# Optimization experiments

Hardware: AMD Instinct MI355X
Metric: run time of the kernel (lower is better)

Reference implementation:

```python
import jax, jax.numpy as jnp
import numpy as np

B, T, D, L, M = 32, 512, 512, 1024, 10


def setup_inputs() -> dict:
    key = jax.random.key(0)
    ks = jax.random.split(key, 9)
    s = 1.0 / np.sqrt(D)  # torch default uniform init bound
    u = lambda k, sh: jax.random.uniform(k, sh, jnp.float32, -s, s)
    return {
        "input_h_c": jax.random.normal(ks[0], (B, T, D), jnp.float32),
        "memory": jax.random.normal(ks[1], (B, L, D), jnp.float32),
        "input_lengths": jax.random.randint(ks[2], (B,), 1, L + 1),
        "W_ih": u(ks[3], (4 * D, 2 * D)),
        "W_hh": u(ks[4], (4 * D, D)),
        "b_ih": u(ks[5], (4 * D,)),
        "b_hh": u(ks[6], (4 * D,)),
        "W_g": u(ks[7], (3 * M, D)),
        "b_g": u(ks[8], (3 * M,)),
    }


def reference(input_h_c, memory, input_lengths, W_ih, W_hh, b_ih, b_hh, W_g, b_g):
    Bq, Tq, Dq = input_h_c.shape
    Lq = memory.shape[1]
    Mq = b_g.shape[0] // 3
    u_pos = jnp.arange(Lq, dtype=memory.dtype)  # [L]

    def step(carry, x_t):
        h, c, ctx, _ = carry
        x = jnp.concatenate([x_t, ctx], axis=-1)  # [B, 2D]
        gates = x @ W_ih.T + b_ih + h @ W_hh.T + b_hh  # [B, 4D]
        i, f, g, o = jnp.split(gates, 4, axis=-1)  # torch LSTMCell gate order i,f,g,o
        c_n = jax.nn.sigmoid(f) * c + jax.nn.sigmoid(i) * jnp.tanh(g)
        h_n = jax.nn.sigmoid(o) * jnp.tanh(c_n)
        # GMM CDF location attention
        phi = h_n @ W_g.T + b_g  # [B, 3M]
        ksi = jnp.exp(phi[:, :Mq])
        beta = jnp.exp(phi[:, Mq:2 * Mq])
        alpha = jax.nn.softmax(phi[:, 2 * Mq:], axis=-1)
        # 1/(1+exp((ksi-u)/beta)) == sigmoid((u-ksi)/beta)
        cdf = lambda ub: jnp.sum(
            alpha[..., None] * jax.nn.sigmoid((ub - ksi[..., None]) / beta[..., None]),
            axis=1)  # [B, L]
        t1 = cdf(u_pos + 0.5)
        w = t1 - cdf(u_pos - 0.5)  # [B, L]
        ctx_n = jnp.einsum('bl,bld->bd', w, memory)
        return (h_n, c_n, ctx_n, 1.0 - t1), w

    z = jnp.zeros((Bq, Dq), input_h_c.dtype)
    term0 = jnp.zeros((Bq, Lq), input_h_c.dtype)
    (h, c, ctx, term), ws = jax.lax.scan(step, (z, z, z, term0),
                                         jnp.swapaxes(input_h_c, 0, 1))
    alignment = jnp.swapaxes(ws, 0, 1)  # [B, T, L]
    termination = jnp.take_along_axis(term, (input_lengths - 1)[:, None], axis=1)  # [B,1]
    return ctx[:, None, :], alignment, termination
```

## Files before the change

kernel.cpp:

```cpp
#include <hip/hip_runtime.h>

#define Bz 32
#define Tz 512
#define Dz 512
#define Lz 1024
#define Mz 10
#define G4D 2048
#define FP 32
#define NBLKA 32
#define NBLK 64
#define OFF_FG   0
#define OFF_FH   1024
#define OFF_FC   2048
#define OFF_SC   3072
#define OFF_SH   11264
#define OFF_PART 19456
#define OFF_XW   84992
#define PM 128
#define PN 128
#define PK 32

typedef unsigned long long u64;
typedef unsigned u32;
typedef _Float16 f16x8 __attribute__((ext_vector_type(8)));
typedef float f32x4 __attribute__((ext_vector_type(4)));
typedef _Float16 half2_t __attribute__((ext_vector_type(2)));

__device__ __forceinline__ float fsig(float x) { return 1.0f / (1.0f + __expf(-x)); }
__device__ __forceinline__ int ld_rlx(const int* p) {
  return __hip_atomic_load(p, __ATOMIC_RELAXED, __HIP_MEMORY_SCOPE_AGENT);
}
__device__ __forceinline__ void st_rlx(int* p, int v) {
  __hip_atomic_store(p, v, __ATOMIC_RELAXED, __HIP_MEMORY_SCOPE_AGENT);
}
__device__ __forceinline__ void st_rlxu(u32* p, u32 v) {
  __hip_atomic_store(p, v, __ATOMIC_RELAXED, __HIP_MEMORY_SCOPE_AGENT);
}
__device__ __forceinline__ u64 ld_rlx64(const u64* p) {
  return __hip_atomic_load(p, __ATOMIC_RELAXED, __HIP_MEMORY_SCOPE_AGENT);
}
__device__ __forceinline__ u32 pack16(float a, float b) {
  unsigned short la = __builtin_bit_cast(unsigned short, (_Float16)a);
  unsigned short lb = __builtin_bit_cast(unsigned short, (_Float16)b);
  return (u32)la | ((u32)lb << 16);
}
#define VWAIT() asm volatile("s_waitcnt vmcnt(0)" ::: "memory")

__global__ __launch_bounds__(256) void k_pre(
    const float* __restrict__ x, const float* __restrict__ W_ih,
    const float* __restrict__ b_ih, const float* __restrict__ b_hh,
    float* __restrict__ xw)
{
  __shared__ float As[PM][PK+1];
  __shared__ float Bs[PN][PK+1];
  const int m0 = blockIdx.x*PM, n0 = blockIdx.y*PN;
  const int tid = threadIdx.x;
  const int mg = tid >> 4, ng = tid & 15;
  float acc[8][8] = {};
  for (int k0 = 0; k0 < Dz; k0 += PK) {
    for (int i = tid; i < PM*(PK/4); i += 256) {
      int row = i >> 3, c4 = (i & 7) << 2;
      float4 v = *reinterpret_cast<const float4*>(&x[(size_t)(m0+row)*Dz + k0 + c4]);
      As[row][c4] = v.x; As[row][c4+1] = v.y; As[row][c4+2] = v.z; As[row][c4+3] = v.w;
    }
    for (int i = tid; i < PN*(PK/4); i += 256) {
      int row = i >> 3, c4 = (i & 7) << 2;
      float4 v = *reinterpret_cast<const float4*>(&W_ih[(size_t)(n0+row)*(2*Dz) + k0 + c4]);
      Bs[row][c4] = v.x; Bs[row][c4+1] = v.y; Bs[row][c4+2] = v.z; Bs[row][c4+3] = v.w;
    }
    __syncthreads();
    #pragma unroll 8
    for (int k = 0; k < PK; k++) {
      float a8[8], b8[8];
      #pragma unroll
      for (int r = 0; r < 8; r++) a8[r] = As[mg*8+r][k];
      #pragma unroll
      for (int s = 0; s < 8; s++) b8[s] = Bs[ng*8+s][k];
      #pragma unroll
      for (int r = 0; r < 8; r++)
        #pragma unroll
        for (int s = 0; s < 8; s++) acc[r][s] += a8[r]*b8[s];
    }
    __syncthreads();
  }
  #pragma unroll
  for (int r = 0; r < 8; r++) {
    int m = m0 + mg*8 + r;
    #pragma unroll
    for (int s = 0; s < 8; s++) {
      int n = n0 + ng*8 + s;
      xw[(size_t)m*G4D + n] = acc[r][s] + b_ih[n] + b_hh[n];
    }
  }
}

__global__ __launch_bounds__(512, 1) void k_persist(
    const float* __restrict__ memory, const int* __restrict__ lens,
    const float* __restrict__ W_ih, const float* __restrict__ W_hh,
    const float* __restrict__ W_g,  const float* __restrict__ b_g,
    const float* __restrict__ xw,
    u32* __restrict__ stat_c, u32* __restrict__ stat_h, u32* __restrict__ part,
    int* __restrict__ fG, int* __restrict__ fH, int* __restrict__ fC,
    float* __restrict__ ctx_out, float* __restrict__ align_out,
    float* __restrict__ term_out)
{
  const int blk = blockIdx.x, tid = threadIdx.x;
  __shared__ __align__(16) char smem[149760];
  __shared__ float phis[3*Mz], prm[3*Mz], lom[Mz], him[Mz];
  __shared__ int rng[2];

  if (blk < NBLKA) {
    const int jt = blk >> 1, kc = blk & 1;
    const int j0 = jt * 128;
    u32* Wl = (u32*)smem;
    u32* xs = (u32*)(smem + 133120);

    for (int i = tid; i < 128*256; i += 512) {
      int jl = i >> 8, ku = i & 255;
      int k = 2*ku;
      float2 wv;
      if (kc == 0) wv = *reinterpret_cast<const float2*>(&W_ih[(size_t)(j0+jl)*(2*Dz) + 512 + k]);
      else         wv = *reinterpret_cast<const float2*>(&W_hh[(size_t)(j0+jl)*Dz + k]);
      Wl[jl*260 + ku] = pack16(wv.x, wv.y);
    }

    const u32* statS = (kc == 0) ? stat_c : stat_h;
    const int* wf    = (kc == 0) ? fC : fH;
    const int w = tid >> 6, lane = tid & 63;
    const int fr = lane & 15;
    const int kq = (lane >> 4) << 2;

    for (int t = 0; t < Tz; ++t) {
      if (t > 0 && tid < Bz) {
        while (ld_rlx(&wf[tid*FP]) < t) __builtin_amdgcn_s_sleep(1);
      }
      __syncthreads();

      #pragma unroll
      for (int h = 0; h < 2; ++h) {
        #pragma unroll
        for (int q = 0; q < 4; ++q) {
          int flat = (q << 9) + tid;
          int bb = flat >> 7, ku2 = flat & 127;
          u64 v = ld_rlx64(reinterpret_cast<const u64*>(statS) + (size_t)(h*16 + bb)*128 + ku2);
          *reinterpret_cast<u64*>(&xs[bb*260 + 2*ku2]) = v;
        }
        __syncthreads();

        f32x4 acc = {0.f, 0.f, 0.f, 0.f};
        const u32* ar = xs + fr*260 + kq;
        const u32* br = Wl + (w*16 + fr)*260 + kq;
        #pragma unroll
        for (int ks = 0; ks < 16; ++ks) {
          f16x8 av = *reinterpret_cast<const f16x8*>(ar + ks*16);
          f16x8 bv = *reinterpret_cast<const f16x8*>(br + ks*16);
          acc = __builtin_amdgcn_mfma_f32_16x16x32_f16(av, bv, acc, 0, 0, 0);
        }
        #pragma unroll
        for (int i = 0; i < 4; ++i) {
          float oth = __shfl_xor(acc[i], 1);
          if (!(lane & 1)) {
            int bg = h*16 + ((lane >> 4) << 2) + i;
            int jc = j0 + w*16 + fr;
            st_rlxu(&part[kc*(Bz*1024) + bg*1024 + (jc >> 1)], pack16(acc[i], oth));
          }
        }
        __syncthreads();
      }
      VWAIT();
      __syncthreads();
      if (tid == 0) st_rlx(&fG[blk*FP], t+1);
    }
    return;
  }

  const int b = blk - NBLKA;
  float* gs   = reinterpret_cast<float*>(smem);
  float* wsm  = reinterpret_cast<float*>(smem + 8192);
  float* hs   = reinterpret_cast<float*>(smem + 12288);
  float* cs   = reinterpret_cast<float*>(smem + 14336);
  float* ctxl = reinterpret_cast<float*>(smem + 16384);
  float* part4 = gs;

  cs[tid] = 0.f;
  __syncthreads();

  for (int t = 0; t < Tz; ++t) {
    float4 xwv = *reinterpret_cast<const float4*>(&xw[((size_t)b*Tz + t)*G4D + 4*tid]);

    if (tid < NBLKA) {
      while (ld_rlx(&fG[tid*FP]) < t+1) __builtin_amdgcn_s_sleep(1);
    }
    __syncthreads();

    {
      u64 p0 = ld_rlx64(reinterpret_cast<const u64*>(part) + (size_t)(0*Bz + b)*512 + tid);
      u64 p1 = ld_rlx64(reinterpret_cast<const u64*>(part) + (size_t)(1*Bz + b)*512 + tid);
      float g0 = xwv.x, g1 = xwv.y, g2v = xwv.z, g3 = xwv.w;
      half2_t l0 = __builtin_bit_cast(half2_t, (u32)p0);
      half2_t h0 = __builtin_bit_cast(half2_t, (u32)(p0 >> 32));
      half2_t l1 = __builtin_bit_cast(half2_t, (u32)p1);
      half2_t h1 = __builtin_bit_cast(half2_t, (u32)(p1 >> 32));
      g0 += (float)l0[0] + (float)l1[0];
      g1 += (float)l0[1] + (float)l1[1];
      g2v += (float)h0[0] + (float)h1[0];
      g3 += (float)h0[1] + (float)h1[1];
      *reinterpret_cast<float4*>(&gs[4*tid]) = make_float4(g0, g1, g2v, g3);
    }
    __syncthreads();

    {
      const int d = tid;
      float ig = 1.0f/(1.0f+expf(-gs[d]));
      float fg = 1.0f/(1.0f+expf(-gs[Dz+d]));
      float gg = tanhf(gs[2*Dz+d]);
      float og = 1.0f/(1.0f+expf(-gs[3*Dz+d]));
      float cn = fg*cs[d] + ig*gg;
      float hn = og*tanhf(cn);
      cs[d] = cn; hs[d] = hn;
    }
    __syncthreads();
    if (tid < 256)
      st_rlxu(&stat_h[b*256 + tid], pack16(hs[2*tid], hs[2*tid+1]));
    VWAIT();
    __syncthreads();
    if (tid == 0) st_rlx(&fH[b*FP], t+1);

    if (tid < 16*3*Mz) {
      int m = tid >> 4, l16 = tid & 15;
      const float4* wr = reinterpret_cast<const float4*>(W_g + m*Dz);
      const float4* hr = reinterpret_cast<const float4*>(hs);
      float s = 0.f;
      #pragma unroll
      for (int i = 0; i < 8; i++) {
        float4 wv = wr[l16 + (i<<4)];
        float4 hv = hr[l16 + (i<<4)];
        s += wv.x*hv.x + wv.y*hv.y + wv.z*hv.z + wv.w*hv.w;
      }
      s += __shfl_xor(s, 1);
      s += __shfl_xor(s, 2);
      s += __shfl_xor(s, 4);
      s += __shfl_xor(s, 8);
      if (l16 == 0) phis[m] = s + b_g[m];
    }
    __syncthreads();

    if (tid < Mz) {
      float ks = expf(phis[tid]);
      float be = expf(phis[Mz + tid]);
      prm[tid]      = ks;
      prm[Mz + tid] = expf(-phis[Mz + tid]);
      lom[tid] = ks - 0.5f - 25.f*be;
      him[tid] = ks + 0.5f + 25.f*be;
    }
    __syncthreads();
    if (tid == 0) {
      float mx = -1e30f;
      #pragma unroll
      for (int m = 0; m < Mz; m++) mx = fmaxf(mx, phis[2*Mz + m]);
      float ae[Mz], ssum = 0.f;
      #pragma unroll
      for (int m = 0; m < Mz; m++) { ae[m] = expf(phis[2*Mz + m] - mx); ssum += ae[m]; }
      float lo = 1e30f, hi = -1e30f;
      #pragma unroll
      for (int m = 0; m < Mz; m++) {
        prm[2*Mz + m] = ae[m] / ssum;
        lo = fminf(lo, lom[m]); hi = fmaxf(hi, him[m]);
      }
      int llo = lo > 0.f ? (int)floorf(lo) : 0;
      if (llo > Lz) llo = Lz;
      int lhi = hi < (float)Lz ? (int)ceilf(hi) + 1 : Lz;
      if (lhi > Lz) lhi = Lz;
      rng[0] = llo; rng[1] = lhi;
    }
    __syncthreads();
    const int llo = rng[0], lhi = rng[1];

    for (int l = llo + tid; l < lhi; l += 512) {
      float u = (float)l;
      float t1 = 0.f, t0 = 0.f;
      #pragma unroll
      for (int m = 0; m < Mz; m++) {
        float ks = prm[m], ib = prm[Mz + m], al = prm[2*Mz + m];
        t1 += al * fsig((u + 0.5f - ks) * ib);
        t0 += al * fsig((u - 0.5f - ks) * ib);
      }
      wsm[l] = t1 - t0;
    }
    __syncthreads();

    {
      const int grp = tid >> 7, d0 = (tid & 127) << 2;
      const float* mb = memory + (size_t)b*Lz*Dz + d0;
      float4 a = make_float4(0.f, 0.f, 0.f, 0.f);
      for (int l = llo + grp; l < lhi; l += 4) {
        float w2 = wsm[l];
        float4 m0 = *reinterpret_cast<const float4*>(&mb[(size_t)l*Dz]);
        a.x = fmaf(w2, m0.x, a.x); a.y = fmaf(w2, m0.y, a.y);
        a.z = fmaf(w2, m0.z, a.z); a.w = fmaf(w2, m0.w, a.w);
      }
      *reinterpret_cast<float4*>(&part4[grp*512 + d0]) = a;
    }
    __syncthreads();
    {
      const int d = tid;
      float s = part4[d] + part4[512 + d] + part4[1024 + d] + part4[1536 + d];
      ctxl[d] = s;
      if (t == Tz-1) ctx_out[b*Dz + d] = s;
    }
    __syncthreads();
    if (tid < 256)
      st_rlxu(&stat_c[b*256 + tid], pack16(ctxl[2*tid], ctxl[2*tid+1]));
    VWAIT();
    __syncthreads();
    if (tid == 0) st_rlx(&fC[b*FP], t+1);

    for (int l = llo + tid; l < lhi; l += 512)
      align_out[((size_t)b*Tz + t)*Lz + l] = wsm[l];
    if (t == Tz-1 && tid == 0) {
      float u = (float)(lens[b] - 1);
      float t1 = 0.f;
      #pragma unroll
      for (int m = 0; m < Mz; m++)
        t1 += prm[2*Mz + m] * fsig((u + 0.5f - prm[m]) * prm[Mz + m]);
      term_out[b] = 1.0f - t1;
    }
  }
}

__global__ __launch_bounds__(256) void k_gemm(
    const float* __restrict__ x_all, const float* __restrict__ ctxs,
    const float* __restrict__ h, const float* __restrict__ W_ih,
    const float* __restrict__ W_hh, float* __restrict__ partial, int t)
{
  __shared__ float Xs[Bz][130];
  __shared__ float Wt[128][130];
  const int jt = blockIdx.x, kcb = blockIdx.y;
  const int j0 = jt*128, k0 = kcb*128;
  const int tid = threadIdx.x;
  for (int i = tid; i < Bz*128; i += 256) {
    int bb = i >> 7, kk = i & 127;
    int k = k0 + kk;
    float v;
    if (k < Dz)        v = x_all[((size_t)bb*Tz + t)*Dz + k];
    else if (k < 2*Dz) v = ctxs[bb*Dz + (k - Dz)];
    else               v = h[bb*Dz + (k - 2*Dz)];
    Xs[bb][kk] = v;
  }
  {
    const float* Wsrc; int ldw, col0;
    if (k0 < 2*Dz) { Wsrc = W_ih; ldw = 2*Dz; col0 = k0; }
    else           { Wsrc = W_hh; ldw = Dz;   col0 = k0 - 2*Dz; }
    for (int i = tid; i < 128*32; i += 256) {
      int jj = i >> 5, k4 = (i & 31) << 2;
      float4 v = *reinterpret_cast<const float4*>(&Wsrc[(size_t)(j0 + jj)*ldw + col0 + k4]);
      Wt[jj][k4] = v.x; Wt[jj][k4+1] = v.y; Wt[jj][k4+2] = v.z; Wt[jj][k4+3] = v.w;
    }
  }
  __syncthreads();
  const int jg = tid & 31, bg = tid >> 5;
  const int bl = bg << 2;
  float acc[4][4] = {};
  #pragma unroll 4
  for (int k = 0; k < 128; k += 2) {
    float2 xv[4], wv[4];
    #pragma unroll
    for (int b2 = 0; b2 < 4; b2++)
      xv[b2] = *reinterpret_cast<const float2*>(&Xs[bl + b2][k]);
    #pragma unroll
    for (int jj = 0; jj < 4; jj++)
      wv[jj] = *reinterpret_cast<const float2*>(&Wt[jg + (jj << 5)][k]);
    #pragma unroll
    for (int jj = 0; jj < 4; jj++)
      #pragma unroll
      for (int b2 = 0; b2 < 4; b2++)
        acc[jj][b2] += wv[jj].x * xv[b2].x + wv[jj].y * xv[b2].y;
  }
  #pragma unroll
  for (int jj = 0; jj < 4; jj++)
    #pragma unroll
    for (int b2 = 0; b2 < 4; b2++)
      partial[((size_t)kcb*Bz + (bl + b2))*G4D + j0 + jg + (jj << 5)] = acc[jj][b2];
}

__global__ __launch_bounds__(512) void k_fused(
    const float* __restrict__ partial, const float* __restrict__ b_ih,
    const float* __restrict__ b_hh,
    float* __restrict__ h, float* __restrict__ c,
    const float* __restrict__ W_g, const float* __restrict__ b_g,
    const float* __restrict__ memory, const int* __restrict__ lens,
    float* __restrict__ ctxs, float* __restrict__ ctx_out,
    float* __restrict__ align_out, float* __restrict__ term_out,
    int t, int final_, int nkc)
{
  const int b = blockIdx.x, tid = threadIdx.x;
  __shared__ float4 gs4[G4D/4];
  __shared__ float hsb[Dz];
  __shared__ float phis[3*Mz];
  __shared__ float prm[3*Mz];
  __shared__ float wsm[Lz];
  __shared__ int   rng[2];
  float* gs = (float*)gs4;
  {
    int j = 4*tid;
    float4 bi = *reinterpret_cast<const float4*>(&b_ih[j]);
    float4 bh = *reinterpret_cast<const float4*>(&b_hh[j]);
    float4 s = make_float4(bi.x+bh.x, bi.y+bh.y, bi.z+bh.z, bi.w+bh.w);
    const float4* pp = reinterpret_cast<const float4*>(partial) + (size_t)b*(G4D/4) + tid;
    for (int kcb = 0; kcb < nkc; kcb++) {
      float4 p = pp[(size_t)kcb*Bz*(G4D/4)];
      s.x += p.x; s.y += p.y; s.z += p.z; s.w += p.w;
    }
    gs4[tid] = s;
  }
  __syncthreads();
  {
    const int d = tid;
    float ig = 1.0f / (1.0f + expf(-gs[d]));
    float fg = 1.0f / (1.0f + expf(-gs[Dz + d]));
    float gg = tanhf(gs[2*Dz + d]);
    float og = 1.0f / (1.0f + expf(-gs[3*Dz + d]));
    float cn = fg * c[b*Dz + d] + ig * gg;
    float hn = og * tanhf(cn);
    c[b*Dz + d] = cn;
    h[b*Dz + d] = hn;
    hsb[d] = hn;
  }
  __syncthreads();
  if (tid < 16*3*Mz) {
    int m = tid >> 4, l16 = tid & 15;
    float s = 0.f;
    #pragma unroll 4
    for (int k = l16; k < Dz; k += 16) s += W_g[m*Dz + k] * hsb[k];
    s += __shfl_xor(s, 1);
    s += __shfl_xor(s, 2);
    s += __shfl_xor(s, 4);
    s += __shfl_xor(s, 8);
    if (l16 == 0) phis[m] = s + b_g[m];
  }
  __syncthreads();
  if (tid == 0) {
    float mx = -1e30f;
    #pragma unroll
    for (int m = 0; m < Mz; m++) mx = fmaxf(mx, phis[2*Mz + m]);
    float ae[Mz], ssum = 0.f;
    #pragma unroll
    for (int m = 0; m < Mz; m++) { ae[m] = expf(phis[2*Mz + m] - mx); ssum += ae[m]; }
    float lo = 1e30f, hi = -1e30f;
    #pragma unroll
    for (int m = 0; m < Mz; m++) {
      float ks = expf(phis[m]);
      float be = expf(phis[Mz + m]);
      prm[m]        = ks;
      prm[Mz + m]   = expf(-phis[Mz + m]);
      prm[2*Mz + m] = ae[m] / ssum;
      lo = fminf(lo, ks - 0.5f - 25.f*be);
      hi = fmaxf(hi, ks + 0.5f + 25.f*be);
    }
    int llo = lo > 0.f ? (int)floorf(lo) : 0;
    if (llo > Lz) llo = Lz;
    int lhi = hi < (float)Lz ? (int)ceilf(hi) + 1 : Lz;
    if (lhi > Lz) lhi = Lz;
    rng[0] = llo; rng[1] = lhi;
  }
  __syncthreads();
  const int llo = rng[0], lhi = rng[1];
  for (int l = llo + tid; l < lhi; l += 512) {
    float u = (float)l;
    float t1 = 0.f, t0 = 0.f;
    #pragma unroll
    for (int m = 0; m < Mz; m++) {
      float ks = prm[m], ib = prm[Mz + m], al = prm[2*Mz + m];
      t1 += al * fsig((u + 0.5f - ks) * ib);
      t0 += al * fsig((u - 0.5f - ks) * ib);
    }
    float w = t1 - t0;
    wsm[l] = w;
    align_out[((size_t)b*Tz + t)*Lz + l] = w;
  }
  __syncthreads();
  {
    const float* mb = memory + (size_t)b*Lz*Dz + tid;
    float acc = 0.f;
    #pragma unroll 4
    for (int l = llo; l < lhi; l++)
      acc += wsm[l] * mb[(size_t)l*Dz];
    ctxs[b*Dz + tid] = acc;
    if (final_) ctx_out[b*Dz + tid] = acc;
  }
  if (final_ && tid == 0) {
    float u = (float)(lens[b] - 1);
    float t1 = 0.f;
    #pragma unroll
    for (int m = 0; m < Mz; m++)
      t1 += prm[2*Mz + m] * fsig((u + 0.5f - prm[m]) * prm[Mz + m]);
    term_out[b] = 1.0f - t1;
  }
}

extern "C" void kernel_launch(void* const* d_in, const int* in_sizes, int n_in,
                              void* d_out, int out_size, void* d_ws, size_t ws_size,
                              hipStream_t stream)
{
  (void)in_sizes; (void)n_in; (void)out_size;
  const float* x    = (const float*)d_in[0];
  const float* mem  = (const float*)d_in[1];
  const int*   lens = (const int*)d_in[2];
  const float* W_ih = (const float*)d_in[3];
  const float* W_hh = (const float*)d_in[4];
  const float* b_ih = (const float*)d_in[5];
  const float* b_hh = (const float*)d_in[6];
  const float* W_g  = (const float*)d_in[7];
  const float* b_g  = (const float*)d_in[8];

  float* out = (float*)d_out;
  float* ctx_out   = out;
  float* align_out = out + Bz*Dz;
  float* term_out  = out + Bz*Dz + (size_t)Bz*Tz*Lz;

  const size_t needP = ((size_t)OFF_XW + (size_t)Bz*Tz*G4D) * sizeof(float);

  hipMemsetAsync(align_out, 0, (size_t)Bz*Tz*Lz*sizeof(float), stream);

  if (ws_size >= needP) {
    int* ip    = (int*)d_ws;
    int* fG    = ip + OFF_FG;
    int* fH    = ip + OFF_FH;
    int* fC    = ip + OFF_FC;
    u32* statc = (u32*)(ip + OFF_SC);
    u32* stath = (u32*)(ip + OFF_SH);
    u32* part  = (u32*)(ip + OFF_PART);
    float* xw  = (float*)(ip + OFF_XW);

    hipMemsetAsync(d_ws, 0, (size_t)OFF_PART * sizeof(int), stream);
    k_pre<<<dim3((Bz*Tz)/PM, G4D/PN), 256, 0, stream>>>(x, W_ih, b_ih, b_hh, xw);
    k_persist<<<NBLK, 512, 0, stream>>>(mem, lens, W_ih, W_hh, W_g, b_g, xw,
                                        statc, stath, part, fG, fH, fC,
                                        ctx_out, align_out, term_out);
  } else {
    float* wsf     = (float*)d_ws;
    float* h       = wsf;
    float* c       = h + Bz*Dz;
    float* ctxs    = c + Bz*Dz;
    float* partial = ctxs + Bz*Dz;
    hipMemsetAsync(d_ws, 0, (size_t)(3*Bz*Dz)*sizeof(float), stream);
    for (int t = 0; t < Tz; t++) {
      k_gemm<<<dim3(G4D/128, 12), 256, 0, stream>>>(x, ctxs, h, W_ih, W_hh, partial, t);
      k_fused<<<Bz, 512, 0, stream>>>(partial, b_ih, b_hh, h, c, W_g, b_g,
                                      mem, lens, ctxs, ctx_out, align_out, term_out,
                                      t, t == Tz-1, 12);
    }
  }
}
```

Measured before the change: 6.794 ms.

## Precompute memory@W_ih_ctx so context gates come from attention weights directly

Uses associativity, ctx@W_ctx^T = w@(memory@W_ctx^T). A new kernel precomputes M2 = memory·W_ih[:,D:]^T per batch in fp16, and the per-step context gate contribution is then formed inside each batch block as a weighted sum over M2 rows. This removes the ctx→GEMM-block round trip and its flag handshake, halving the GEMM blocks to only W_hh. The xw precompute is also stored as fp16 and LDS tiles get an XOR swizzle. The trade-offs are reading 2048 fp16 values per memory row instead of 512 floats in the per-step reduction, a large extra workspace, and reduced precision.

```diff
diff --git a/kernel.cpp b/kernel.cpp
--- a/kernel.cpp
+++ b/kernel.cpp
@@ -7,15 +7,15 @@
 #define Mz 10
 #define G4D 2048
 #define FP 32
-#define NBLKA 32
-#define NBLK 64
+#define NBLKA 16
+#define NBLK  48
 #define OFF_FG   0
-#define OFF_FH   1024
-#define OFF_FC   2048
-#define OFF_SC   3072
-#define OFF_SH   11264
-#define OFF_PART 19456
-#define OFF_XW   84992
+#define OFF_FH   512
+#define OFF_SH   1536
+#define OFF_PART 9728
+#define OFF_M2   42496
+#define OFF_XW   33596928
+#define NEED_I   50374144
 #define PM 128
 #define PN 128
 #define PK 32
@@ -44,12 +44,18 @@
   unsigned short lb = __builtin_bit_cast(unsigned short, (_Float16)b);
   return (u32)la | ((u32)lb << 16);
 }
+__device__ __forceinline__ float lo16(u32 v) {
+  return (float)__builtin_bit_cast(half2_t, v)[0];
+}
+__device__ __forceinline__ float hi16(u32 v) {
+  return (float)__builtin_bit_cast(half2_t, v)[1];
+}
 #define VWAIT() asm volatile("s_waitcnt vmcnt(0)" ::: "memory")
 
 __global__ __launch_bounds__(256) void k_pre(
     const float* __restrict__ x, const float* __restrict__ W_ih,
     const float* __restrict__ b_ih, const float* __restrict__ b_hh,
-    float* __restrict__ xw)
+    u32* __restrict__ xwu)
 {
   __shared__ float As[PM][PK+1];
   __shared__ float Bs[PN][PK+1];
@@ -83,24 +89,74 @@
     }
     __syncthreads();
   }
+  const int nb = n0 + ng*8;
   #pragma unroll
   for (int r = 0; r < 8; r++) {
     int m = m0 + mg*8 + r;
     #pragma unroll
-    for (int s = 0; s < 8; s++) {
-      int n = n0 + ng*8 + s;
-      xw[(size_t)m*G4D + n] = acc[r][s] + b_ih[n] + b_hh[n];
-    }
+    for (int s2 = 0; s2 < 4; s2++) {
+      int n = nb + 2*s2;
+      xwu[(size_t)m*1024 + (n >> 1)] =
+          pack16(acc[r][2*s2]   + b_ih[n]   + b_hh[n],
+                 acc[r][2*s2+1] + b_ih[n+1] + b_hh[n+1]);
+    }
+  }
+}
+
+__global__ __launch_bounds__(512) void k_m2(
+    const float* __restrict__ memory, const float* __restrict__ W_ih,
+    u32* __restrict__ M2u)
+{
+  __shared__ __align__(16) u32 smem[149760/4];
+  u32* Bs = smem;
+  u32* As = smem + 33280;
+  const int tid = threadIdx.x;
+  const int n0 = blockIdx.x * 128, mc = blockIdx.y;
+  for (int i = tid; i < 128*256; i += 512) {
+    int jl = i >> 8, ku = i & 255;
+    float2 wv = *reinterpret_cast<const float2*>(&W_ih[(size_t)(n0+jl)*(2*Dz) + 512 + 2*ku]);
+    Bs[jl*260 + (ku ^ ((jl & 7) << 2))] = pack16(wv.x, wv.y);
+  }
+  __syncthreads();
+  const int w = tid >> 6, lane = tid & 63;
+  const int fr = lane & 15, kq = (lane >> 4) << 2;
+  const int frsw = (fr & 7) << 2;
+  for (int mt = 0; mt < 128; ++mt) {
+    const int m0 = mc*2048 + mt*16;
+    for (int i = tid; i < 16*256; i += 512) {
+      int r = i >> 8, ku = i & 255;
+      float2 mv = *reinterpret_cast<const float2*>(&memory[(size_t)(m0+r)*Dz + 2*ku]);
+      As[r*260 + (ku ^ ((r & 7) << 2))] = pack16(mv.x, mv.y);
+    }
+    __syncthreads();
+    f32x4 acc = {0.f, 0.f, 0.f, 0.f};
+    #pragma unroll
+    for (int ks = 0; ks < 16; ++ks) {
+      int col = (kq + ks*16) ^ frsw;
+      f16x8 av = *reinterpret_cast<const f16x8*>(As + fr*260 + col);
+      f16x8 bv = *reinterpret_cast<const f16x8*>(Bs + (w*16 + fr)*260 + col);
+      acc = __builtin_amdgcn_mfma_f32_16x16x32_f16(av, bv, acc, 0, 0, 0);
+    }
+    #pragma unroll
+    for (int i = 0; i < 4; ++i) {
+      float oth = __shfl_xor(acc[i], 1);
+      if (!(lane & 1)) {
+        int m = m0 + ((lane >> 4) << 2) + i;
+        int j = n0 + w*16 + fr;
+        M2u[(size_t)m*1024 + (j >> 1)] = pack16(acc[i], oth);
+      }
+    }
+    __syncthreads();
   }
 }
 
 __global__ __launch_bounds__(512, 1) void k_persist(
     const float* __restrict__ memory, const int* __restrict__ lens,
-    const float* __restrict__ W_ih, const float* __restrict__ W_hh,
-    const float* __restrict__ W_g,  const float* __restrict__ b_g,
-    const float* __restrict__ xw,
-    u32* __restrict__ stat_c, u32* __restrict__ stat_h, u32* __restrict__ part,
-    int* __restrict__ fG, int* __restrict__ fH, int* __restrict__ fC,
+    const float* __restrict__ W_hh, const float* __restrict__ W_g,
+    const float* __restrict__ b_g,
+    const u32* __restrict__ xwu, const u32* __restrict__ M2u,
+    u32* __restrict__ stat_h, u32* __restrict__ part,
+    int* __restrict__ fG, int* __restrict__ fH,
     float* __restrict__ ctx_out, float* __restrict__ align_out,
     float* __restrict__ term_out)
 {
@@ -110,59 +166,52 @@
   __shared__ int rng[2];
 
   if (blk < NBLKA) {
-    const int jt = blk >> 1, kc = blk & 1;
-    const int j0 = jt * 128;
+    const int j0 = blk * 128;
     u32* Wl = (u32*)smem;
     u32* xs = (u32*)(smem + 133120);
 
     for (int i = tid; i < 128*256; i += 512) {
       int jl = i >> 8, ku = i & 255;
-      int k = 2*ku;
-      float2 wv;
-      if (kc == 0) wv = *reinterpret_cast<const float2*>(&W_ih[(size_t)(j0+jl)*(2*Dz) + 512 + k]);
-      else         wv = *reinterpret_cast<const float2*>(&W_hh[(size_t)(j0+jl)*Dz + k]);
-      Wl[jl*260 + ku] = pack16(wv.x, wv.y);
-    }
-
-    const u32* statS = (kc == 0) ? stat_c : stat_h;
-    const int* wf    = (kc == 0) ? fC : fH;
+      float2 wv = *reinterpret_cast<const float2*>(&W_hh[(size_t)(j0+jl)*Dz + 2*ku]);
+      Wl[jl*260 + (ku ^ ((jl & 7) << 2))] = pack16(wv.x, wv.y);
+    }
+
     const int w = tid >> 6, lane = tid & 63;
-    const int fr = lane & 15;
-    const int kq = (lane >> 4) << 2;
+    const int fr = lane & 15, kq = (lane >> 4) << 2;
+    const int frsw = (fr & 7) << 2;
 
     for (int t = 0; t < Tz; ++t) {
       if (t > 0 && tid < Bz) {
-        while (ld_rlx(&wf[tid*FP]) < t) __builtin_amdgcn_s_sleep(1);
+        while (ld_rlx(&fH[tid*FP]) < t) __builtin_amdgcn_s_sleep(1);
       }
       __syncthreads();
 
       #pragma unroll
-      for (int h = 0; h < 2; ++h) {
+      for (int hh = 0; hh < 2; ++hh) {
         #pragma unroll
         for (int q = 0; q < 4; ++q) {
           int flat = (q << 9) + tid;
           int bb = flat >> 7, ku2 = flat & 127;
-          u64 v = ld_rlx64(reinterpret_cast<const u64*>(statS) + (size_t)(h*16 + bb)*128 + ku2);
-          *reinterpret_cast<u64*>(&xs[bb*260 + 2*ku2]) = v;
+          u64 v = ld_rlx64(reinterpret_cast<const u64*>(stat_h) + (size_t)(hh*16 + bb)*128 + ku2);
+          *reinterpret_cast<u64*>(&xs[bb*260 + ((2*ku2) ^ ((bb & 7) << 2))]) = v;
         }
         __syncthreads();
 
         f32x4 acc = {0.f, 0.f, 0.f, 0.f};
-        const u32* ar = xs + fr*260 + kq;
-        const u32* br = Wl + (w*16 + fr)*260 + kq;
         #pragma unroll
         for (int ks = 0; ks < 16; ++ks) {
-          f16x8 av = *reinterpret_cast<const f16x8*>(ar + ks*16);
-          f16x8 bv = *reinterpret_cast<const f16x8*>(br + ks*16);
+          int col = (kq + ks*16) ^ frsw;
+          f16x8 av = *reinterpret_cast<const f16x8*>(xs + fr*260 + col);
+          f16x8 bv = *reinterpret_cast<const f16x8*>(Wl + (w*16 + fr)*260 + col);
           acc = __builtin_amdgcn_mfma_f32_16x16x32_f16(av, bv, acc, 0, 0, 0);
         }
         #pragma unroll
         for (int i = 0; i < 4; ++i) {
           float oth = __shfl_xor(acc[i], 1);
           if (!(lane & 1)) {
-            int bg = h*16 + ((lane >> 4) << 2) + i;
+            int bg = hh*16 + ((lane >> 4) << 2) + i;
             int jc = j0 + w*16 + fr;
-            st_rlxu(&part[kc*(Bz*1024) + bg*1024 + (jc >> 1)], pack16(acc[i], oth));
+            st_rlxu(&part[bg*1024 + (jc >> 1)], pack16(acc[i], oth));
           }
         }
         __syncthreads();
@@ -176,17 +225,19 @@
 
   const int b = blk - NBLKA;
   float* gs   = reinterpret_cast<float*>(smem);
-  float* wsm  = reinterpret_cast<float*>(smem + 8192);
-  float* hs   = reinterpret_cast<float*>(smem + 12288);
-  float* cs   = reinterpret_cast<float*>(smem + 14336);
-  float* ctxl = reinterpret_cast<float*>(smem + 16384);
+  float* gctx = reinterpret_cast<float*>(smem + 8192);
+  float* wsm  = reinterpret_cast<float*>(smem + 16384);
+  float* hs   = reinterpret_cast<float*>(smem + 20480);
+  float* cs   = reinterpret_cast<float*>(smem + 22528);
   float* part4 = gs;
 
   cs[tid] = 0.f;
+  #pragma unroll
+  for (int q = 0; q < 4; ++q) gctx[(q << 9) + tid] = 0.f;
   __syncthreads();
 
   for (int t = 0; t < Tz; ++t) {
-    float4 xwv = *reinterpret_cast<const float4*>(&xw[((size_t)b*Tz + t)*G4D + 4*tid]);
+    u64 xv = *(reinterpret_cast<const u64*>(xwu) + ((size_t)(b*Tz + t) << 9) + tid);
 
     if (tid < NBLKA) {
       while (ld_rlx(&fG[tid*FP]) < t+1) __builtin_amdgcn_s_sleep(1);
@@ -194,18 +245,14 @@
     __syncthreads();
 
     {
-      u64 p0 = ld_rlx64(reinterpret_cast<const u64*>(part) + (size_t)(0*Bz + b)*512 + tid);
-      u64 p1 = ld_rlx64(reinterpret_cast<const u64*>(part) + (size_t)(1*Bz + b)*512 + tid);
-      float g0 = xwv.x, g1 = xwv.y, g2v = xwv.z, g3 = xwv.w;
-      half2_t l0 = __builtin_bit_cast(half2_t, (u32)p0);
-      half2_t h0 = __builtin_bit_cast(half2_t, (u32)(p0 >> 32));
-      half2_t l1 = __builtin_bit_cast(half2_t, (u32)p1);
-      half2_t h1 = __builtin_bit_cast(half2_t, (u32)(p1 >> 32));
-      g0 += (float)l0[0] + (float)l1[0];
-      g1 += (float)l0[1] + (float)l1[1];
-      g2v += (float)h0[0] + (float)h1[0];
-      g3 += (float)h0[1] + (float)h1[1];
-      *reinterpret_cast<float4*>(&gs[4*tid]) = make_float4(g0, g1, g2v, g3);
+      u64 pv = ld_rlx64(reinterpret_cast<const u64*>(part) + (size_t)b*512 + tid);
+      u32 x0 = (u32)xv, x1 = (u32)(xv >> 32);
+      u32 p0 = (u32)pv, p1 = (u32)(pv >> 32);
+      float g0 = lo16(x0) + lo16(p0) + gctx[4*tid];
+      float g1 = hi16(x0) + hi16(p0) + gctx[4*tid+1];
+      float g2 = lo16(x1) + lo16(p1) + gctx[4*tid+2];
+      float g3 = hi16(x1) + hi16(p1) + gctx[4*tid+3];
+      *reinterpret_cast<float4*>(&gs[4*tid]) = make_float4(g0, g1, g2, g3);
     }
     __syncthreads();
 
@@ -289,42 +336,47 @@
     }
     __syncthreads();
 
-    {
-      const int grp = tid >> 7, d0 = (tid & 127) << 2;
-      const float* mb = memory + (size_t)b*Lz*Dz + d0;
-      float4 a = make_float4(0.f, 0.f, 0.f, 0.f);
-      for (int l = llo + grp; l < lhi; l += 4) {
-        float w2 = wsm[l];
-        float4 m0 = *reinterpret_cast<const float4*>(&mb[(size_t)l*Dz]);
-        a.x = fmaf(w2, m0.x, a.x); a.y = fmaf(w2, m0.y, a.y);
-        a.z = fmaf(w2, m0.z, a.z); a.w = fmaf(w2, m0.w, a.w);
-      }
-      *reinterpret_cast<float4*>(&part4[grp*512 + d0]) = a;
-    }
-    __syncthreads();
-    {
-      const int d = tid;
-      float s = part4[d] + part4[512 + d] + part4[1024 + d] + part4[1536 + d];
-      ctxl[d] = s;
-      if (t == Tz-1) ctx_out[b*Dz + d] = s;
-    }
-    __syncthreads();
-    if (tid < 256)
-      st_rlxu(&stat_c[b*256 + tid], pack16(ctxl[2*tid], ctxl[2*tid+1]));
-    VWAIT();
-    __syncthreads();
-    if (tid == 0) st_rlx(&fC[b*FP], t+1);
+    if (t < Tz-1) {
+      float a0 = 0.f, a1 = 0.f, a2 = 0.f, a3 = 0.f;
+      const u64* m2r = reinterpret_cast<const u64*>(M2u) + ((size_t)(b << 10) << 9) + tid;
+      for (int l = llo; l < lhi; ++l) {
+        float wl = wsm[l];
+        u64 v = m2r[(size_t)l << 9];
+        u32 v0 = (u32)v, v1 = (u32)(v >> 32);
+        a0 = fmaf(wl, lo16(v0), a0);
+        a1 = fmaf(wl, hi16(v0), a1);
+        a2 = fmaf(wl, lo16(v1), a2);
+        a3 = fmaf(wl, hi16(v1), a3);
+      }
+      *reinterpret_cast<float4*>(&gctx[4*tid]) = make_float4(a0, a1, a2, a3);
+    } else {
+      __syncthreads();
+      {
+        const int grp = tid >> 7, d0 = (tid & 127) << 2;
+        const float* mb = memory + (size_t)b*Lz*Dz + d0;
+        float4 a = make_float4(0.f, 0.f, 0.f, 0.f);
+        for (int l = llo + grp; l < lhi; l += 4) {
+          float wl = wsm[l];
+          float4 m0 = *reinterpret_cast<const float4*>(&mb[(size_t)l*Dz]);
+          a.x = fmaf(wl, m0.x, a.x); a.y = fmaf(wl, m0.y, a.y);
+          a.z = fmaf(wl, m0.z, a.z); a.w = fmaf(wl, m0.w, a.w);
+        }
+        *reinterpret_cast<float4*>(&part4[grp*512 + d0]) = a;
+      }
+      __syncthreads();
+      ctx_out[b*Dz + tid] = part4[tid] + part4[512 + tid] + part4[1024 + tid] + part4[1536 + tid];
+      if (tid == 0) {
+        float u = (float)(lens[b] - 1);
+        float t1 = 0.f;
+        #pragma unroll
+        for (int m = 0; m < Mz; m++)
+          t1 += prm[2*Mz + m] * fsig((u + 0.5f - prm[m]) * prm[Mz + m]);
+        term_out[b] = 1.0f - t1;
+      }
+    }
 
     for (int l = llo + tid; l < lhi; l += 512)
       align_out[((size_t)b*Tz + t)*Lz + l] = wsm[l];
-    if (t == Tz-1 && tid == 0) {
-      float u = (float)(lens[b] - 1);
-      float t1 = 0.f;
-      #pragma unroll
-      for (int m = 0; m < Mz; m++)
-        t1 += prm[2*Mz + m] * fsig((u + 0.5f - prm[m]) * prm[Mz + m]);
-      term_out[b] = 1.0f - t1;
-    }
   }
 }
 
@@ -518,7 +570,7 @@
   float* align_out = out + Bz*Dz;
   float* term_out  = out + Bz*Dz + (size_t)Bz*Tz*Lz;
 
-  const size_t needP = ((size_t)OFF_XW + (size_t)Bz*Tz*G4D) * sizeof(float);
+  const size_t needP = (size_t)NEED_I * sizeof(int);
 
   hipMemsetAsync(align_out, 0, (size_t)Bz*Tz*Lz*sizeof(float), stream);
 
@@ -526,16 +578,16 @@
     int* ip    = (int*)d_ws;
     int* fG    = ip + OFF_FG;
     int* fH    = ip + OFF_FH;
-    int* fC    = ip + OFF_FC;
-    u32* statc = (u32*)(ip + OFF_SC);
     u32* stath = (u32*)(ip + OFF_SH);
     u32* part  = (u32*)(ip + OFF_PART);
-    float* xw  = (float*)(ip + OFF_XW);
-
-    hipMemsetAsync(d_ws, 0, (size_t)OFF_PART * sizeof(int), stream);
-    k_pre<<<dim3((Bz*Tz)/PM, G4D/PN), 256, 0, stream>>>(x, W_ih, b_ih, b_hh, xw);
-    k_persist<<<NBLK, 512, 0, stream>>>(mem, lens, W_ih, W_hh, W_g, b_g, xw,
-                                        statc, stath, part, fG, fH, fC,
+    u32* M2u   = (u32*)(ip + OFF_M2);
+    u32* xwu   = (u32*)(ip + OFF_XW);
+
+    hipMemsetAsync(d_ws, 0, (size_t)OFF_M2 * sizeof(int), stream);
+    k_pre<<<dim3((Bz*Tz)/PM, G4D/PN), 256, 0, stream>>>(x, W_ih, b_ih, b_hh, xwu);
+    k_m2<<<dim3(16, 16), 512, 0, stream>>>(mem, W_ih, M2u);
+    k_persist<<<NBLK, 512, 0, stream>>>(mem, lens, W_hh, W_g, b_g, xwu, M2u,
+                                        stath, part, fG, fH,
                                         ctx_out, align_out, term_out);
   } else {
     float* wsf     = (float*)d_ws;
```

Result: faster. 6.628 ms (-2.4%).
